# Kernel tuning notes

Measured on AMD Instinct MI355X. Metric: run time of the kernel, lower is better.

Reference implementation:

```python
import jax, jax.numpy as jnp
import numpy as np

B, S, A, H, N = 4096, 128, 32, 1024, 256
BETA = 1.0            # params['temperature']
NORM_SMOOTHING = 0.01 # params['norm_smoothing']
MAX_A = 1.0           # env.action_space.high[0]
# dropout_rate = 0.0 and eval-mode reference -> dropout is identity


def setup_inputs() -> dict:
    key = jax.random.key(0)
    ks = jax.random.split(key, 16)
    sc_s = 1.0 / np.sqrt(S)
    sc_h = 1.0 / np.sqrt(H)
    return {
        "s": jax.random.normal(ks[0], (B, S), jnp.float32),
        "a": jax.random.normal(ks[1], (B, A), jnp.float32),
        # value side MLP: S->H->H->H->N
        "Wv1": jax.random.uniform(ks[2], (S, H), jnp.float32, -sc_s, sc_s),
        "bv1": jax.random.uniform(ks[3], (H,), jnp.float32, -sc_s, sc_s),
        "Wv2": jax.random.uniform(ks[4], (H, H), jnp.float32, -sc_h, sc_h),
        "bv2": jax.random.uniform(ks[5], (H,), jnp.float32, -sc_h, sc_h),
        "Wv3": jax.random.uniform(ks[6], (H, H), jnp.float32, -sc_h, sc_h),
        "bv3": jax.random.uniform(ks[7], (H,), jnp.float32, -sc_h, sc_h),
        "Wv4": jax.random.uniform(ks[8], (H, N), jnp.float32, -sc_h, sc_h),
        "bv4": jax.random.uniform(ks[9], (N,), jnp.float32, -sc_h, sc_h),
        # location side: S->H (xavier), then N expert linears H->A stacked
        "Wl1": jax.random.normal(ks[10], (S, H), jnp.float32) * np.sqrt(2.0 / (S + H)),
        "bl1": jnp.zeros((H,), jnp.float32),
        "Wexp": jax.random.uniform(ks[11], (N, H, A), jnp.float32, -0.1, 0.1),
        "bexp": jax.random.uniform(ks[12], (N, A), jnp.float32, -1.0, 1.0),
    }


def reference(s, a, Wv1, bv1, Wv2, bv2, Wv3, bv3, Wv4, bv4, Wl1, bl1, Wexp, bexp):
    t = jax.nn.relu(s @ Wv1 + bv1)
    t = jax.nn.relu(t @ Wv2 + bv2)
    t = jax.nn.relu(t @ Wv3 + bv3)
    values = t @ Wv4 + bv4                      # [B, N]

    # --- get_all_centroids: shared hidden, N expert heads as grouped GEMM ---
    h = jax.nn.relu(s @ Wl1 + bl1)              # [B, H] (dropout identity)
    centroids = MAX_A * jnp.tanh(
        jnp.einsum("bh,nha->bna", h, Wexp) + bexp[None]
    )                                           # [B, N, A]

    # --- rbf_function: softmax over -beta * ||centroid - a|| ---
    diff = centroids - a[:, None, :]            # [B, N, A]
    dist = jnp.sqrt(jnp.sum(diff * diff, axis=2) + NORM_SMOOTHING)  # [B, N]
    weights = jax.nn.softmax(-BETA * dist, axis=1)                  # [B, N]

    return jnp.sum(weights * values, axis=1, keepdims=True)         # [B, 1]
```

## Files before the change

### kernel.cpp

```cpp
#include <hip/hip_runtime.h>
#include <hip/hip_bf16.h>


typedef _Float16 half8 __attribute__((ext_vector_type(8)));
typedef _Float16 half4v __attribute__((ext_vector_type(4)));
typedef float floatx16 __attribute__((ext_vector_type(16)));

namespace {
constexpr int kB = 4096, kS = 128, kA = 32, kH = 1024, kN = 256;
constexpr size_t al(size_t x) { return (x + 255) & ~size_t(255); }
constexpr size_t OFF_FLAG  = 0;
constexpr size_t OFF_S16   = 256;
constexpr size_t OFF_WEXPT = OFF_S16   + al((size_t)kB * kS * 2);
constexpr size_t OFF_WV1T  = OFF_WEXPT + al((size_t)kN * kA * kH * 2);
constexpr size_t OFF_WL1T  = OFF_WV1T  + (size_t)kS * kH * 2;
constexpr size_t OFF_WV2T  = OFF_WL1T  + al((size_t)kS * kH * 2);
constexpr size_t OFF_WV3T  = OFF_WV2T  + al((size_t)kH * kH * 2);
constexpr size_t OFF_WV4T  = OFF_WV3T  + al((size_t)kH * kH * 2);
constexpr size_t OFF_BUFC  = OFF_WV4T  + al((size_t)kH * kN * 2);
constexpr size_t OFF_B2V   = OFF_BUFC  + al((size_t)kB * 2 * kH * 2);
constexpr size_t OFF_B3    = OFF_B2V   + al((size_t)kB * kH * 2);
constexpr size_t OFF_VAL   = OFF_B3    + al((size_t)kB * kH * 2);
constexpr size_t OFF_DIST  = OFF_VAL   + al((size_t)kB * kN * 4);
}

__device__ __forceinline__ float ldraw(const void* p, size_t i, int bf) {
    if (bf) return __uint_as_float(((unsigned)((const unsigned short*)p)[i]) << 16);
    return ((const float*)p)[i];
}

__device__ __forceinline__ float4 ldraw4(const void* p, size_t i, int bf) {
    if (bf) {
        ushort4 u = *(const ushort4*)((const unsigned short*)p + i);
        return make_float4(__uint_as_float((unsigned)u.x << 16),
                           __uint_as_float((unsigned)u.y << 16),
                           __uint_as_float((unsigned)u.z << 16),
                           __uint_as_float((unsigned)u.w << 16));
    }
    return *(const float4*)((const float*)p + i);
}

__device__ __forceinline__ void gl_lds16(const _Float16* g, _Float16* l) {
    __builtin_amdgcn_global_load_lds(
        (const __attribute__((address_space(1))) unsigned int*)g,
        (__attribute__((address_space(3))) unsigned int*)l, 16, 0, 0);
}

template <int N>
__device__ __forceinline__ void waitcnt_vm() {
    if constexpr (N == 0)      asm volatile("s_waitcnt vmcnt(0)" ::: "memory");
    else if constexpr (N == 2) asm volatile("s_waitcnt vmcnt(2)" ::: "memory");
    else if constexpr (N == 4) asm volatile("s_waitcnt vmcnt(4)" ::: "memory");
    else if constexpr (N == 6) asm volatile("s_waitcnt vmcnt(6)" ::: "memory");
    else if constexpr (N == 8) asm volatile("s_waitcnt vmcnt(8)" ::: "memory");
    else if constexpr (N == 16) asm volatile("s_waitcnt vmcnt(16)" ::: "memory");
    else static_assert(N == 0, "unsupported vmcnt");
}
__device__ __forceinline__ void lgkm0() { asm volatile("s_waitcnt lgkmcnt(0)" ::: "memory"); }

__device__ __forceinline__ float fast_tanh(float x) {
    x = fminf(9.f, fmaxf(-9.f, x));
    float e = __expf(2.f * x);
    return (e - 1.f) * __builtin_amdgcn_rcpf(e + 1.f);
}

__global__ void detect_kernel(const unsigned int* __restrict__ s_raw, int* __restrict__ flag) {
    __shared__ int cnt;
    if (threadIdx.x == 0) cnt = 0;
    __syncthreads();
    const unsigned e = (s_raw[threadIdx.x] >> 7) & 0xFFu;
    int c = (e >= 118u && e <= 135u) ? 1 : 0;
    for (int off = 32; off > 0; off >>= 1) c += __shfl_down(c, off);
    if ((threadIdx.x & 63) == 0) atomicAdd(&cnt, c);
    __syncthreads();
    if (threadIdx.x == 0) *flag = (cnt > 128) ? 1 : 0;
}

struct TDesc { const void* src; _Float16* dst; int K; int N; int tiles; };
struct TPack { TDesc d[7]; };

__global__ void transpose_all(TPack p, const int* __restrict__ flag) {
    __shared__ float tile[32][33];
    const int bf = *flag;
    int bid = blockIdx.x;
    int i = 0;
    while (bid >= p.d[i].tiles) { bid -= p.d[i].tiles; ++i; }
    const void* src = p.d[i].src;
    _Float16* dst = p.d[i].dst;
    const int tx = threadIdx.x, ty = threadIdx.y;
    const int K = p.d[i].K, N = p.d[i].N;
    if (K == 0) {
        const int lin = ty * 8 + tx;
        const size_t base = (size_t)bid * 4096;
#pragma unroll
        for (int t = 0; t < 4; ++t) {
            const size_t idx = base + (size_t)t * 1024 + (size_t)lin * 4;
            float4 v = ldraw4(src, idx, bf);
            half4v o = {(_Float16)v.x, (_Float16)v.y, (_Float16)v.z, (_Float16)v.w};
            *(half4v*)(dst + idx) = o;
        }
        return;
    }
    const int tpz = (N >> 5) * (K >> 5);
    const int z = bid / tpz, r = bid - z * tpz;
    const int n0 = (r % (N >> 5)) * 32, k0 = (r / (N >> 5)) * 32;
    const size_t zo = (size_t)z * K * N;
    float4 v = ldraw4(src, zo + (size_t)(k0 + ty) * N + n0 + tx * 4, bf);
    tile[ty][tx * 4 + 0] = v.x;
    tile[ty][tx * 4 + 1] = v.y;
    tile[ty][tx * 4 + 2] = v.z;
    tile[ty][tx * 4 + 3] = v.w;
    __syncthreads();
    half4v o;
#pragma unroll
    for (int j = 0; j < 4; ++j) o[j] = (_Float16)tile[tx * 4 + j][ty];
    *(half4v*)(dst + zo + (size_t)(n0 + ty) * K + k0 + tx * 4) = o;
}

struct GArgs {
    const _Float16* A;
    const _Float16* Bt;
    const void* bias;
    const void* bias2;
    void* C;
    const void* a_raw;
    float* dist;
    int split;
    int N, K, lda, Mt, Nt, relu, of16, fuse;
};

template <int TM, int TN, int WM, int WN>
__device__ __forceinline__ void dgemm_core(const GArgs& g, int bid, const int* flagp) {
    constexpr int NT = WM * WN * 64;
    constexpr int BK = 32;
    constexpr int NST = 4;
    constexpr int MI = TM / WM / 32, NI = TN / WN / 32;
    constexpr int ACH = TM * BK / 8;
    constexpr int BCH = TN * BK / 8;
    constexpr int AT = (ACH + NT - 1) / NT;
    constexpr int BT = (BCH + NT - 1) / NT;
    constexpr int LPS = AT + BT;
    __shared__ _Float16 As[NST * ACH * 8];
    __shared__ _Float16 Bs[NST * BCH * 8];

    const int tid = threadIdx.x;
    const int lane = tid & 63;
    const int w = tid >> 6, wr = w / WN, wc = w % WN;
    const int N = g.N, K = g.K, lda = g.lda;

    int mt, nt;
    if ((g.Mt & 7) == 0 && (g.Nt & 7) == 0) {
        const int xcd = bid & 7, loc = bid >> 3;
        const int Bn = g.Nt >> 3;
        const int sr = loc / (8 * Bn);
        const int rem = loc - sr * (8 * Bn);
        mt = sr * 8 + (rem & 7);
        nt = xcd * Bn + (rem >> 3);
    } else {
        mt = bid % g.Mt;
        nt = bid / g.Mt;
    }
    const int m0 = mt * TM, n0 = nt * TN;

    const _Float16* gAsrc[AT];
    _Float16* lAdst[AT];
#pragma unroll
    for (int t = 0; t < AT; ++t) {
        int c = t * NT + tid;
        if (c >= ACH) c = ACH - 1;
        const int ks = c / (TM * 2), rem = c % (TM * 2);
        const int row = (rem >> 6) * 32 + (rem & 31);
        const int kcol = ks * 16 + ((rem >> 5) & 1) * 8;
        gAsrc[t] = g.A + (size_t)(m0 + row) * lda + kcol;
        lAdst[t] = As + c * 8;
    }
    const _Float16* gBsrc[BT];
    _Float16* lBdst[BT];
#pragma unroll
    for (int t = 0; t < BT; ++t) {
        int c = t * NT + tid;
        if (c >= BCH) c = BCH - 1;
        const int ks = c / (TN * 2), rem = c % (TN * 2);
        const int row = (rem >> 6) * 32 + (rem & 31);
        const int kcol = ks * 16 + ((rem >> 5) & 1) * 8;
        gBsrc[t] = g.Bt + (size_t)(n0 + row) * K + kcol;
        lBdst[t] = Bs + c * 8;
    }

    auto issue = [&](int k0, int st) {
#pragma unroll
        for (int t = 0; t < AT; ++t)
            if ((t + 1) * NT <= ACH || t * NT + tid < ACH)
                gl_lds16(gAsrc[t] + k0, lAdst[t] + st * ACH * 8);
#pragma unroll
        for (int t = 0; t < BT; ++t)
            if ((t + 1) * NT <= BCH || t * NT + tid < BCH)
                gl_lds16(gBsrc[t] + k0, lBdst[t] + st * BCH * 8);
    };

    floatx16 acc[MI][NI];
#pragma unroll
    for (int mi = 0; mi < MI; ++mi)
#pragma unroll
        for (int ni = 0; ni < NI; ++ni)
#pragma unroll
            for (int i = 0; i < 16; ++i) acc[mi][ni][i] = 0.f;

    auto compute = [&](int st) {
        const int ao = st * ACH * 8, bo = st * BCH * 8;
#pragma unroll
        for (int ks = 0; ks < 2; ++ks) {
            half8 af[MI], bf[NI];
#pragma unroll
            for (int mi = 0; mi < MI; ++mi)
                af[mi] = *(const half8*)(As + ao + ((size_t)(ks * TM * 2 + (wr * MI + mi) * 64 + lane)) * 8);
#pragma unroll
            for (int ni = 0; ni < NI; ++ni)
                bf[ni] = *(const half8*)(Bs + bo + ((size_t)(ks * TN * 2 + (wc * NI + ni) * 64 + lane)) * 8);
#pragma unroll
            for (int mi = 0; mi < MI; ++mi)
#pragma unroll
                for (int ni = 0; ni < NI; ++ni)
                    acc[mi][ni] = __builtin_amdgcn_mfma_f32_32x32x16_f16(af[mi], bf[ni], acc[mi][ni], 0, 0, 0);
        }
    };

    const int ntiles = K / BK;
    issue(0, 0);
    if (ntiles > 1) issue(BK, 1);
    if (ntiles > 2) issue(2 * BK, 2);
    for (int kt = 0; kt < ntiles; ++kt) {
        const int rem = ntiles - 1 - kt;
        if (rem >= 2)      waitcnt_vm<2 * LPS>();
        else if (rem == 1) waitcnt_vm<LPS>();
        else               waitcnt_vm<0>();
        __builtin_amdgcn_s_barrier();
        asm volatile("" ::: "memory");
        __builtin_amdgcn_sched_barrier(0);
        if (kt + 3 < ntiles) issue((kt + 3) * BK, (kt + 3) & 3);
        __builtin_amdgcn_s_setprio(1);
        compute(kt & 3);
        __builtin_amdgcn_s_setprio(0);
        lgkm0();
    }

    const int bf_ = *flagp;
    const int am = lane & 31;
    const int half = lane >> 5;

    if (g.fuse) {
        const int ebase = n0 >> 5;
        float bvv[NI];
#pragma unroll
        for (int ni = 0; ni < NI; ++ni)
            bvv[ni] = ldraw(g.bias, (size_t)(n0 + (wc * NI + ni) * 32 + am), bf_);
        float* a_s = (float*)As;
        float* d_s = (float*)Bs;
        __syncthreads();
        for (int idx = tid; idx < TM * kA; idx += NT)
            a_s[idx] = ldraw(g.a_raw, (size_t)(m0 + (idx >> 5)) * kA + (idx & 31), bf_);
        __syncthreads();
#pragma unroll
        for (int mi = 0; mi < MI; ++mi)
#pragma unroll
            for (int rr = 0; rr < 16; ++rr) {
                const int row_loc = (wr * MI + mi) * 32 + (rr & 3) + 8 * (rr >> 2) + 4 * half;
                const float av = a_s[row_loc * kA + am];
#pragma unroll
                for (int ni = 0; ni < NI; ++ni) {
                    const float c = fast_tanh(acc[mi][ni][rr] + bvv[ni]);
                    const float d = c - av;
                    float d2 = d * d;
                    d2 += __shfl_xor(d2, 1);
                    d2 += __shfl_xor(d2, 2);
                    d2 += __shfl_xor(d2, 4);
                    d2 += __shfl_xor(d2, 8);
                    d2 += __shfl_xor(d2, 16);
                    if (am == 0) d_s[row_loc * 8 + wc * NI + ni] = d2;
                }
            }
        __syncthreads();
        for (int idx = tid; idx < TM * 8; idx += NT)
            g.dist[(size_t)(m0 + (idx >> 3)) * kN + ebase + (idx & 7)] = sqrtf(d_s[idx] + 0.01f);
        return;
    }

#pragma unroll
    for (int mi = 0; mi < MI; ++mi)
#pragma unroll
        for (int ni = 0; ni < NI; ++ni) {
            const int Rb = m0 + (wr * MI + mi) * 32;
            const int Cb = n0 + (wc * NI + ni) * 32 + am;
            const float bv = (Cb < g.split) ? ldraw(g.bias, Cb, bf_)
                                            : ldraw(g.bias2, Cb - g.split, bf_);
#pragma unroll
            for (int rr = 0; rr < 16; ++rr) {
                const int row = Rb + (rr & 3) + 8 * (rr >> 2) + 4 * half;
                float x = acc[mi][ni][rr] + bv;
                if (g.relu) x = fmaxf(x, 0.f);
                if (g.of16) ((_Float16*)g.C)[(size_t)row * N + Cb] = (_Float16)x;
                else ((float*)g.C)[(size_t)row * N + Cb] = x;
            }
        }
}

template <int TM, int TN, int WM, int WN>
__launch_bounds__(WM * WN * 64, 2)
__global__ void dgemm_one(GArgs g, const int* __restrict__ flagp) {
    dgemm_core<TM, TN, WM, WN>(g, blockIdx.x, flagp);
}

__launch_bounds__(256)
__global__ void final_softmax(const float* __restrict__ dist, const float* __restrict__ values,
                              const int* __restrict__ flag, void* __restrict__ out) {
    const int row = blockIdx.x * 4 + (threadIdx.x >> 6);
    const int lane = threadIdx.x & 63;
    const float4 d4 = *(const float4*)(dist + (size_t)row * kN + lane * 4);
    const float4 v4 = *(const float4*)(values + (size_t)row * kN + lane * 4);
    float m = fminf(fminf(d4.x, d4.y), fminf(d4.z, d4.w));
#pragma unroll
    for (int off = 32; off > 0; off >>= 1) m = fminf(m, __shfl_xor(m, off));
    const float w0 = expf(m - d4.x), w1 = expf(m - d4.y);
    const float w2 = expf(m - d4.z), w3 = expf(m - d4.w);
    float ws = (w0 + w1) + (w2 + w3);
    float wv = fmaf(w0, v4.x, fmaf(w1, v4.y, fmaf(w2, v4.z, w3 * v4.w)));
#pragma unroll
    for (int off = 32; off > 0; off >>= 1) {
        ws += __shfl_xor(ws, off);
        wv += __shfl_xor(wv, off);
    }
    if (lane == 0) {
        const float o = wv / ws;
        if (*flag) ((__hip_bfloat16*)out)[row] = __float2bfloat16(o);
        else       ((float*)out)[row] = o;
    }
}

extern "C" void kernel_launch(void* const* d_in, const int* in_sizes, int n_in,
                              void* d_out, int out_size, void* d_ws, size_t ws_size,
                              hipStream_t stream) {
    (void)in_sizes; (void)n_in; (void)out_size; (void)ws_size;
    char* ws = (char*)d_ws;
    int* flag = (int*)(ws + OFF_FLAG);
    _Float16* s16   = (_Float16*)(ws + OFF_S16);
    _Float16* wexpt = (_Float16*)(ws + OFF_WEXPT);
    _Float16* wv1t  = (_Float16*)(ws + OFF_WV1T);
    _Float16* wl1t  = (_Float16*)(ws + OFF_WL1T);
    _Float16* wv2t  = (_Float16*)(ws + OFF_WV2T);
    _Float16* wv3t  = (_Float16*)(ws + OFF_WV3T);
    _Float16* wv4t  = (_Float16*)(ws + OFF_WV4T);
    _Float16* bufC  = (_Float16*)(ws + OFF_BUFC);
    _Float16* b2v   = (_Float16*)(ws + OFF_B2V);
    _Float16* b3    = (_Float16*)(ws + OFF_B3);
    float* values   = (float*)(ws + OFF_VAL);
    float* distb    = (float*)(ws + OFF_DIST);

    detect_kernel<<<1, 256, 0, stream>>>((const unsigned int*)d_in[0], flag);

    TPack tp;
    tp.d[0] = {d_in[2],  wv1t,  kS, kH, (kH / 32) * (kS / 32)};
    tp.d[1] = {d_in[10], wl1t,  kS, kH, (kH / 32) * (kS / 32)};
    tp.d[2] = {d_in[4],  wv2t,  kH, kH, (kH / 32) * (kH / 32)};
    tp.d[3] = {d_in[6],  wv3t,  kH, kH, (kH / 32) * (kH / 32)};
    tp.d[4] = {d_in[8],  wv4t,  kH, kN, (kN / 32) * (kH / 32)};
    tp.d[5] = {d_in[12], wexpt, kH, kA, kN * (kA / 32) * (kH / 32)};
    tp.d[6] = {d_in[0],  s16,   0,  kB * kS, (kB * kS) / 4096};
    int total_tiles = 0;
    for (int i = 0; i < 7; ++i) total_tiles += tp.d[i].tiles;
    transpose_all<<<total_tiles, dim3(8, 32), 0, stream>>>(tp, flag);

    const int BIG = 1 << 30;
    {
        GArgs g{s16, wv1t, d_in[3], d_in[11], bufC, nullptr, nullptr, kH,
                2 * kH, kS, kS, kB / 64, (2 * kH) / 64, 1, 1, 0};
        dgemm_one<64, 64, 2, 2><<<(kB / 64) * ((2 * kH) / 64), 256, 0, stream>>>(g, flag);
    }
    {
        GArgs g{bufC, wv2t, d_in[5], d_in[5], b2v, nullptr, nullptr, BIG,
                kH, kH, 2 * kH, kB / 128, kH / 128, 1, 1, 0};
        dgemm_one<128, 128, 2, 2><<<(kB / 128) * (kH / 128), 256, 0, stream>>>(g, flag);
    }
    {
        GArgs g{b2v, wv3t, d_in[7], d_in[7], b3, nullptr, nullptr, BIG,
                kH, kH, kH, kB / 128, kH / 128, 1, 1, 0};
        dgemm_one<128, 128, 2, 2><<<(kB / 128) * (kH / 128), 256, 0, stream>>>(g, flag);
    }
    {
        GArgs g{b3, wv4t, d_in[9], d_in[9], values, nullptr, nullptr, BIG,
                kN, kH, kH, kB / 64, kN / 64, 0, 0, 0};
        dgemm_one<64, 64, 2, 2><<<(kB / 64) * (kN / 64), 256, 0, stream>>>(g, flag);
    }
    {
        GArgs g{bufC + kH, wexpt, d_in[13], d_in[13], nullptr, d_in[1], distb,
                BIG, kN * kA, kH, 2 * kH, kB / 256, (kN * kA) / 256, 0, 0, 1};
        dgemm_one<256, 256, 2, 4><<<(kB / 256) * ((kN * kA) / 256), 512, 0, stream>>>(g, flag);
    }
    final_softmax<<<kB / 4, 256, 0, stream>>>(distb, values, flag, d_out);
}
```

Before: 377.7 us.

## Use 16-wave blocks with double-buffered LDS pipeline for expert GEMM

Adds an NST template parameter and a two-stage pipelined main loop with an extra barrier before refilling a buffer. The expert-head GEMM now uses 4x4 waves (1024 threads) and two LDS stages, halving shared memory use and per-thread accumulators. The aim is to raise latency hiding and occupancy for the largest GEMM. The costs are a shallower prefetch, which can expose memory latency, and register pressure from the 1024-thread launch bound.

```diff
diff --git a/kernel.cpp b/kernel.cpp
--- a/kernel.cpp
+++ b/kernel.cpp
@@ -129,11 +129,10 @@
     int N, K, lda, Mt, Nt, relu, of16, fuse;
 };
 
-template <int TM, int TN, int WM, int WN>
+template <int TM, int TN, int WM, int WN, int NST>
 __device__ __forceinline__ void dgemm_core(const GArgs& g, int bid, const int* flagp) {
     constexpr int NT = WM * WN * 64;
     constexpr int BK = 32;
-    constexpr int NST = 4;
     constexpr int MI = TM / WM / 32, NI = TN / WN / 32;
     constexpr int ACH = TM * BK / 8;
     constexpr int BCH = TN * BK / 8;
@@ -226,22 +225,40 @@
     };
 
     const int ntiles = K / BK;
-    issue(0, 0);
-    if (ntiles > 1) issue(BK, 1);
-    if (ntiles > 2) issue(2 * BK, 2);
-    for (int kt = 0; kt < ntiles; ++kt) {
-        const int rem = ntiles - 1 - kt;
-        if (rem >= 2)      waitcnt_vm<2 * LPS>();
-        else if (rem == 1) waitcnt_vm<LPS>();
-        else               waitcnt_vm<0>();
-        __builtin_amdgcn_s_barrier();
-        asm volatile("" ::: "memory");
-        __builtin_amdgcn_sched_barrier(0);
-        if (kt + 3 < ntiles) issue((kt + 3) * BK, (kt + 3) & 3);
-        __builtin_amdgcn_s_setprio(1);
-        compute(kt & 3);
-        __builtin_amdgcn_s_setprio(0);
-        lgkm0();
+    if constexpr (NST == 2) {
+        issue(0, 0);
+        if (ntiles > 1) issue(BK, 1);
+        for (int kt = 0; kt < ntiles; ++kt) {
+            if (kt + 1 < ntiles) waitcnt_vm<LPS>();
+            else                 waitcnt_vm<0>();
+            __builtin_amdgcn_s_barrier();
+            asm volatile("" ::: "memory");
+            __builtin_amdgcn_sched_barrier(0);
+            __builtin_amdgcn_s_setprio(1);
+            compute(kt & 1);
+            __builtin_amdgcn_s_setprio(0);
+            lgkm0();
+            __builtin_amdgcn_s_barrier();
+            if (kt + 2 < ntiles) issue((kt + 2) * BK, kt & 1);
+        }
+    } else {
+        issue(0, 0);
+        if (ntiles > 1) issue(BK, 1);
+        if (ntiles > 2) issue(2 * BK, 2);
+        for (int kt = 0; kt < ntiles; ++kt) {
+            const int rem = ntiles - 1 - kt;
+            if (rem >= 2)      waitcnt_vm<2 * LPS>();
+            else if (rem == 1) waitcnt_vm<LPS>();
+            else               waitcnt_vm<0>();
+            __builtin_amdgcn_s_barrier();
+            asm volatile("" ::: "memory");
+            __builtin_amdgcn_sched_barrier(0);
+            if (kt + 3 < ntiles) issue((kt + 3) * BK, (kt + 3) & 3);
+            __builtin_amdgcn_s_setprio(1);
+            compute(kt & 3);
+            __builtin_amdgcn_s_setprio(0);
+            lgkm0();
+        }
     }
 
     const int bf_ = *flagp;
@@ -304,10 +321,10 @@
         }
 }
 
-template <int TM, int TN, int WM, int WN>
+template <int TM, int TN, int WM, int WN, int NST>
 __launch_bounds__(WM * WN * 64, 2)
 __global__ void dgemm_one(GArgs g, const int* __restrict__ flagp) {
-    dgemm_core<TM, TN, WM, WN>(g, blockIdx.x, flagp);
+    dgemm_core<TM, TN, WM, WN, NST>(g, blockIdx.x, flagp);
 }
 
 __launch_bounds__(256)
@@ -373,27 +390,27 @@
     {
         GArgs g{s16, wv1t, d_in[3], d_in[11], bufC, nullptr, nullptr, kH,
                 2 * kH, kS, kS, kB / 64, (2 * kH) / 64, 1, 1, 0};
-        dgemm_one<64, 64, 2, 2><<<(kB / 64) * ((2 * kH) / 64), 256, 0, stream>>>(g, flag);
+        dgemm_one<64, 64, 2, 2, 4><<<(kB / 64) * ((2 * kH) / 64), 256, 0, stream>>>(g, flag);
     }
     {
         GArgs g{bufC, wv2t, d_in[5], d_in[5], b2v, nullptr, nullptr, BIG,
                 kH, kH, 2 * kH, kB / 128, kH / 128, 1, 1, 0};
-        dgemm_one<128, 128, 2, 2><<<(kB / 128) * (kH / 128), 256, 0, stream>>>(g, flag);
+        dgemm_one<128, 128, 2, 2, 4><<<(kB / 128) * (kH / 128), 256, 0, stream>>>(g, flag);
     }
     {
         GArgs g{b2v, wv3t, d_in[7], d_in[7], b3, nullptr, nullptr, BIG,
                 kH, kH, kH, kB / 128, kH / 128, 1, 1, 0};
-        dgemm_one<128, 128, 2, 2><<<(kB / 128) * (kH / 128), 256, 0, stream>>>(g, flag);
+        dgemm_one<128, 128, 2, 2, 4><<<(kB / 128) * (kH / 128), 256, 0, stream>>>(g, flag);
     }
     {
         GArgs g{b3, wv4t, d_in[9], d_in[9], values, nullptr, nullptr, BIG,
                 kN, kH, kH, kB / 64, kN / 64, 0, 0, 0};
-        dgemm_one<64, 64, 2, 2><<<(kB / 64) * (kN / 64), 256, 0, stream>>>(g, flag);
+        dgemm_one<64, 64, 2, 2, 4><<<(kB / 64) * (kN / 64), 256, 0, stream>>>(g, flag);
     }
     {
         GArgs g{bufC + kH, wexpt, d_in[13], d_in[13], nullptr, d_in[1], distb,
                 BIG, kN * kA, kH, 2 * kH, kB / 256, (kN * kA) / 256, 0, 0, 1};
-        dgemm_one<256, 256, 2, 4><<<(kB / 256) * ((kN * kA) / 256), 512, 0, stream>>>(g, flag);
+        dgemm_one<256, 256, 4, 4, 2><<<(kB / 256) * ((kN * kA) / 256), 1024, 0, stream>>>(g, flag);
     }
     final_softmax<<<kB / 4, 256, 0, stream>>>(distb, values, flag, d_out);
 }
```

New measurement: 343.8 us. 9.0% less time.
